# Kernel optimization log

Hardware: AMD Instinct MI355X
Metric: run time of the kernel (lower is better)

Reference implementation:

```python
import jax, jax.numpy as jnp
import numpy as np

B, T, N, E = 8, 32, 128, 2048
IN_DIM, HID, OUT = 512, 512, 512
SLOPE = 0.2  # GATConv default negative_slope


def setup_inputs() -> dict:
    key = jax.random.key(0)
    ks = jax.random.split(key, 12)
    x = jax.random.normal(ks[0], (B, T, N, IN_DIM), jnp.float32)
    edge_index = jax.random.randint(ks[1], (B, T, 2, E), 0, N)
    valid_step_index = jax.random.randint(ks[2], (B,), 1, T + 1)
    def lin(k, o, i):
        return jax.random.normal(k, (o, i), jnp.float32) / np.sqrt(i).astype(np.float32)
    W1 = lin(ks[3], HID, IN_DIM)
    a1_src = jax.random.normal(ks[4], (HID,), jnp.float32) / np.sqrt(HID).astype(np.float32)
    a1_dst = jax.random.normal(ks[5], (HID,), jnp.float32) / np.sqrt(HID).astype(np.float32)
    b1 = jnp.zeros((HID,), jnp.float32)
    W2 = lin(ks[6], OUT, HID)
    a2_src = jax.random.normal(ks[7], (OUT,), jnp.float32) / np.sqrt(OUT).astype(np.float32)
    a2_dst = jax.random.normal(ks[8], (OUT,), jnp.float32) / np.sqrt(OUT).astype(np.float32)
    b2 = jnp.zeros((OUT,), jnp.float32)
    W_time = jax.random.normal(ks[9], (T, T), jnp.float32) / np.sqrt(T).astype(np.float32)
    b_time = jnp.zeros((T,), jnp.float32)
    return dict(x=x, edge_index=edge_index, valid_step_index=valid_step_index,
                W1=W1, a1_src=a1_src, a1_dst=a1_dst, b1=b1,
                W2=W2, a2_src=a2_src, a2_dst=a2_dst, b2=b2,
                W_time=W_time, b_time=b_time)


def _gat(x, src, dst, W, a_src, a_dst, b):
    # Single-head PyG GATConv (concat=True, heads=1), self-loops already appended.
    n = x.shape[0]
    h = x @ W.T                                             # [N, H]
    e = jax.nn.leaky_relu((h @ a_src)[src] + (h @ a_dst)[dst], SLOPE)  # [E]
    m = jax.ops.segment_max(e, dst, num_segments=n)
    m = jnp.where(jnp.isfinite(m), m, 0.0)
    p = jnp.exp(e - m[dst])
    denom = jax.ops.segment_sum(p, dst, num_segments=n)
    alpha = p / denom[dst]                                  # segment softmax over incoming edges
    return jax.ops.segment_sum(h[src] * alpha[:, None], dst, num_segments=n) + b


def reference(x, edge_index, valid_step_index, W1, a1_src, a1_dst, b1,
              W2, a2_src, a2_dst, b2, W_time, b_time):
    b_, t_, n_, _ = x.shape
    g = b_ * t_
    xf = x.reshape(g, n_, -1)
    ei = edge_index.reshape(g, 2, -1)
    # add self loops (PyG GATConv default add_self_loops=True)
    loops = jnp.broadcast_to(jnp.arange(n_)[None, None, :], (g, 2, n_))
    ei = jnp.concatenate([ei, loops], axis=-1)
    src, dst = ei[:, 0], ei[:, 1]
    gat = jax.vmap(_gat, in_axes=(0, 0, 0, None, None, None, None))
    h = jax.nn.gelu(gat(xf, src, dst, W1, a1_src, a1_dst, b1), approximate=False)
    # F.dropout(p=0.2) is identity in eval mode
    h = gat(h, src, dst, W2, a2_src, a2_dst, b2)
    y = h.reshape(b_, t_, n_, -1)
    mask = (jnp.arange(t_)[None, :] < valid_step_index[:, None]).astype(y.dtype)
    y = y * mask[:, :, None, None]
    # TemporalConv: Conv2d(T, T, 1) over time-as-channel = linear mix across time, then GELU, residual
    fused = jax.nn.gelu(jnp.einsum('ts,bsnf->btnf', W_time, y)
                        + b_time[None, :, None, None], approximate=False)
    return fused + y
```

## Files before the change

kernel.cpp:

```cpp
#include <hip/hip_runtime.h>

using u16 = unsigned short;
using u32 = unsigned int;

typedef __bf16 bf16x8 __attribute__((ext_vector_type(8)));
typedef float  f32x4  __attribute__((ext_vector_type(4)));

__device__ __forceinline__ u16 f2bf(float f) {
    u32 u = __float_as_uint(f);
    u32 r = u + 0x7fffu + ((u >> 16) & 1u);
    return (u16)(r >> 16);
}
__device__ __forceinline__ float gelu_f(float x) {
    return 0.5f * x * (1.0f + erff(x * 0.70710678118654752440f));
}

#define GLOAD16(gp, lp) __builtin_amdgcn_global_load_lds( \
    (const __attribute__((address_space(1))) void*)(gp),  \
    (__attribute__((address_space(3))) void*)(lp), 16, 0, 0)

__global__ __launch_bounds__(256) void prep_kernel(
    const float* __restrict__ x, u16* __restrict__ Xb, float* __restrict__ Z)
{
    const int i0 = blockIdx.x * 256 + threadIdx.x;
    const int stride = gridDim.x * 256;
    if (i0 < 32768) ((float4*)Z)[i0] = make_float4(0.f, 0.f, 0.f, 0.f);
    for (int i = i0; i < 4194304; i += stride) {
        float4 v = ((const float4*)x)[i];
        ushort4 o;
        o.x = f2bf(v.x); o.y = f2bf(v.y); o.z = f2bf(v.z); o.w = f2bf(v.w);
        ((ushort4*)Xb)[i] = o;
    }
}

__global__ __launch_bounds__(512) void gat_gemm(
    const u16* __restrict__ A, const float* __restrict__ W,
    const float* __restrict__ a_s, const float* __restrict__ a_d,
    u16* __restrict__ HT, float* __restrict__ SS, float* __restrict__ SD)
{
    __shared__ __align__(16) u16 As[2][128 * 32];
    __shared__ float sA[128], dA[128];

    const int tid  = threadIdx.x;
    const int lane = tid & 63;
    const int w    = tid >> 6;
    const int rl   = lane & 15;
    const int grp  = lane >> 4;
    const int g    = blockIdx.x >> 1;
    const int hf   = blockIdx.x & 1;

    if (tid < 128) { sA[tid] = 0.f; dA[tid] = 0.f; }

    const u16* Ag   = A + (size_t)g * 65536;
    const u16* asrc = Ag + (size_t)(w * 16 + (lane >> 2)) * 512 + (lane & 3) * 8;
    const float* wg = W + (size_t)(hf * 256 + w * 32 + rl) * 512 + grp * 8;

    float4 wf0[2], wf1[2];
    wf0[0] = *(const float4*)&wg[0];     wf1[0] = *(const float4*)&wg[4];
    wf0[1] = *(const float4*)&wg[8192];  wf1[1] = *(const float4*)&wg[8192 + 4];

    GLOAD16(asrc, &As[0][w * 512]);
    __syncthreads();

    f32x4 acc[8][2] = {};
    int buf = 0;
    for (int kt = 0; kt < 16; ++kt) {
        if (kt < 15) GLOAD16(asrc + (kt + 1) * 32, &As[buf ^ 1][w * 512]);
        bf16x8 wb[2];
        #pragma unroll
        for (int j = 0; j < 2; ++j) {
            float4 lo = wf0[j], hi = wf1[j];
            wb[j][0] = (__bf16)lo.x; wb[j][1] = (__bf16)lo.y;
            wb[j][2] = (__bf16)lo.z; wb[j][3] = (__bf16)lo.w;
            wb[j][4] = (__bf16)hi.x; wb[j][5] = (__bf16)hi.y;
            wb[j][6] = (__bf16)hi.z; wb[j][7] = (__bf16)hi.w;
        }
        if (kt < 15) {
            #pragma unroll
            for (int j = 0; j < 2; ++j) {
                wf0[j] = *(const float4*)&wg[j * 8192 + (kt + 1) * 32];
                wf1[j] = *(const float4*)&wg[j * 8192 + (kt + 1) * 32 + 4];
            }
        }
        #pragma unroll
        for (int i = 0; i < 8; ++i) {
            bf16x8 af = *(const bf16x8*)&As[buf][(i * 16 + rl) * 32 + grp * 8];
            acc[i][0] = __builtin_amdgcn_mfma_f32_16x16x32_bf16(af, wb[0], acc[i][0], 0, 0, 0);
            acc[i][1] = __builtin_amdgcn_mfma_f32_16x16x32_bf16(af, wb[1], acc[i][1], 0, 0, 0);
        }
        __syncthreads();
        buf ^= 1;
    }

    float asv[2], adv[2];
    #pragma unroll
    for (int j = 0; j < 2; ++j) {
        int f = hf * 256 + w * 32 + j * 16 + rl;
        asv[j] = a_s[f]; adv[j] = a_d[f];
    }
    u16* Hg = HT + (size_t)g * 65536;
    #pragma unroll
    for (int i = 0; i < 8; ++i) {
        #pragma unroll
        for (int j = 0; j < 2; ++j) {
            int f = hf * 256 + w * 32 + j * 16 + rl;
            int node0 = i * 16 + grp * 4;
            ushort4 o;
            o.x = f2bf(acc[i][j][0]); o.y = f2bf(acc[i][j][1]);
            o.z = f2bf(acc[i][j][2]); o.w = f2bf(acc[i][j][3]);
            *(ushort4*)&Hg[(size_t)f * 128 + node0] = o;
        }
        #pragma unroll
        for (int r = 0; r < 4; ++r) {
            float s = acc[i][0][r] * asv[0] + acc[i][1][r] * asv[1];
            float d = acc[i][0][r] * adv[0] + acc[i][1][r] * adv[1];
            #pragma unroll
            for (int off = 1; off < 16; off <<= 1) {
                s += __shfl_xor(s, off);
                d += __shfl_xor(d, off);
            }
            if (rl == 0) {
                int node = i * 16 + grp * 4 + r;
                atomicAdd(&sA[node], s);
                atomicAdd(&dA[node], d);
            }
        }
    }
    __syncthreads();
    if (tid < 128) {
        atomicAdd(&SS[g * 128 + tid], sA[tid]);
        atomicAdd(&SD[g * 128 + tid], dA[tid]);
    }
}

template<int MODE>
__global__ __launch_bounds__(512) void gat_agg(
    const u16* __restrict__ HT, const int* __restrict__ ei,
    const float* __restrict__ SS, const float* __restrict__ SD,
    const float* __restrict__ bias, const int* __restrict__ valid,
    u16* __restrict__ outU, float* __restrict__ outF)
{
    __shared__ u16 Hts[65536];
    __shared__ u32 cntw[2048];
    __shared__ float stf[512];

    const int tid  = threadIdx.x;
    const int lane = tid & 63;
    const int w    = tid >> 6;
    const int rl   = lane & 15;
    const int grp  = lane >> 4;
    const int g    = blockIdx.x;
    const int bb   = g >> 5, tt = g & 31;

    const int4* es = (const int4*)(ei + (size_t)g * 4096);
    int4 e0 = es[tid], e1 = es[512 + tid];

    const u16* Hg = HT + (size_t)g * 65536;
    #pragma unroll
    for (int it = 0; it < 16; ++it) {
        int f = it * 32 + (tid >> 4);
        int blk = tid & 15;
        GLOAD16(Hg + (size_t)f * 128 + ((blk ^ (f & 15)) * 8), &Hts[it * 4096 + w * 512]);
    }

    for (int i = tid; i < 2048; i += 512) cntw[i] = 0u;
    if (tid < 128) {
        stf[tid]       = SS[g * 128 + tid];
        stf[128 + tid] = SD[g * 128 + tid];
    }
    __syncthreads();

    atomicAdd(&cntw[e1.x * 16 + (e0.x >> 3)], 1u << ((e0.x & 7) * 4));
    atomicAdd(&cntw[e1.y * 16 + (e0.y >> 3)], 1u << ((e0.y & 7) * 4));
    atomicAdd(&cntw[e1.z * 16 + (e0.z >> 3)], 1u << ((e0.z & 7) * 4));
    atomicAdd(&cntw[e1.w * 16 + (e0.w >> 3)], 1u << ((e0.w & 7) * 4));
    if (tid < 128) atomicAdd(&cntw[tid * 16 + (tid >> 3)], 1u << ((tid & 7) * 4));
    __syncthreads();

    for (int r = 0; r < 16; ++r) {
        int m = w * 16 + r;
        float sdm = stf[128 + m];
        u32 w0 = cntw[m * 16 + (lane >> 3)];
        u32 w1 = cntw[m * 16 + 8 + (lane >> 3)];
        u32 c0 = (w0 >> ((lane & 7) * 4)) & 15u;
        u32 c1 = (w1 >> ((lane & 7) * 4)) & 15u;
        float E0 = stf[lane] + sdm;      E0 = E0 > 0.f ? E0 : 0.2f * E0;
        float E1 = stf[lane + 64] + sdm; E1 = E1 > 0.f ? E1 : 0.2f * E1;
        float mx = fmaxf(c0 ? E0 : -1e30f, c1 ? E1 : -1e30f);
        #pragma unroll
        for (int off = 1; off < 64; off <<= 1) mx = fmaxf(mx, __shfl_xor(mx, off));
        float p = (c0 ? (float)c0 * __expf(E0 - mx) : 0.f)
                + (c1 ? (float)c1 * __expf(E1 - mx) : 0.f);
        #pragma unroll
        for (int off = 1; off < 64; off <<= 1) p += __shfl_xor(p, off);
        if (lane == 0) { stf[256 + m] = mx; stf[384 + m] = 1.f / p; }
    }
    __syncthreads();

    const int m = w * 16 + rl;
    const float sdm = stf[128 + m], Mm = stf[256 + m], rDm = stf[384 + m];
    bf16x8 pa[4];
    #pragma unroll
    for (int kb = 0; kb < 4; ++kb) {
        u32 word = cntw[m * 16 + kb * 4 + grp];
        #pragma unroll
        for (int e = 0; e < 8; ++e) {
            u32 c = (word >> (e * 4)) & 15u;
            int s = kb * 32 + grp * 8 + e;
            float ev = stf[s] + sdm; ev = ev > 0.f ? ev : 0.2f * ev;
            float p = c ? (float)c * __expf(ev - Mm) * rDm : 0.f;
            pa[kb][e] = (__bf16)p;
        }
    }

    const float msk = (MODE == 1) ? ((tt < valid[bb]) ? 1.f : 0.f) : 1.f;
    #pragma unroll 1
    for (int jc = 0; jc < 8; ++jc) {
        f32x4 acc2[4] = {};
        #pragma unroll
        for (int j4 = 0; j4 < 4; ++j4) {
            int f = jc * 64 + j4 * 16 + rl;
            #pragma unroll
            for (int kb = 0; kb < 4; ++kb) {
                bf16x8 hb = *(const bf16x8*)&Hts[f * 128 + (((kb * 4 + grp) ^ (f & 15)) * 8)];
                acc2[j4] = __builtin_amdgcn_mfma_f32_16x16x32_bf16(pa[kb], hb, acc2[j4], 0, 0, 0);
            }
        }
        #pragma unroll
        for (int j4 = 0; j4 < 4; ++j4) {
            int f = jc * 64 + j4 * 16 + rl;
            float bv = bias[f];
            #pragma unroll
            for (int r = 0; r < 4; ++r) {
                int m2 = w * 16 + grp * 4 + r;
                if (MODE == 0)
                    outU[(size_t)g * 65536 + m2 * 512 + f] = f2bf(gelu_f(acc2[j4][r] + bv));
                else
                    outF[(size_t)g * 65536 + m2 * 512 + f] = (acc2[j4][r] + bv) * msk;
            }
        }
    }
}

__global__ __launch_bounds__(256) void timemix_kernel(float* __restrict__ y,
                                                      const float* __restrict__ Wt,
                                                      const float* __restrict__ bt) {
    __shared__ float wsm[1024];
    __shared__ float bts[32];
    int tid = threadIdx.x;
    for (int i = tid; i < 1024; i += 256) wsm[i] = Wt[i];
    if (tid < 32) bts[tid] = bt[tid];
    __syncthreads();
    int blk = blockIdx.x;
    int b = blk >> 8;
    int rem = blk & 255;
    int n = rem >> 1;
    int f = (rem & 1) * 256 + tid;
    size_t base = ((size_t)b * 4096 + n) * 512 + f;
    float ys[32];
    #pragma unroll
    for (int s = 0; s < 32; ++s) ys[s] = y[base + (size_t)s * 65536];
    #pragma unroll
    for (int t = 0; t < 32; ++t) {
        float a = bts[t];
        #pragma unroll
        for (int s = 0; s < 32; ++s) a += wsm[t * 32 + s] * ys[s];
        y[base + (size_t)t * 65536] = gelu_f(a) + ys[t];
    }
}

extern "C" void kernel_launch(void* const* d_in, const int* in_sizes, int n_in,
                              void* d_out, int out_size, void* d_ws, size_t ws_size,
                              hipStream_t stream) {
    const float* x     = (const float*)d_in[0];
    const int*   ei    = (const int*)d_in[1];
    const int*   valid = (const int*)d_in[2];
    const float* W1    = (const float*)d_in[3];
    const float* a1s   = (const float*)d_in[4];
    const float* a1d   = (const float*)d_in[5];
    const float* b1    = (const float*)d_in[6];
    const float* W2    = (const float*)d_in[7];
    const float* a2s   = (const float*)d_in[8];
    const float* a2d   = (const float*)d_in[9];
    const float* b2    = (const float*)d_in[10];
    const float* Wt    = (const float*)d_in[11];
    const float* bt    = (const float*)d_in[12];
    float* out = (float*)d_out;

    char* ws = (char*)d_ws;
    u16* Xb    = (u16*)(ws);
    u16* HTb   = (u16*)(ws + 33554432);
    float* SS1 = (float*)(ws + 67108864);
    float* SD1 = (float*)(ws + 67239936);
    float* SS2 = (float*)(ws + 67371008);
    float* SD2 = (float*)(ws + 67502080);

    prep_kernel<<<2048, 256, 0, stream>>>(x, Xb, SS1);

    gat_gemm<<<512, 512, 0, stream>>>(Xb, W1, a1s, a1d, HTb, SS1, SD1);
    gat_agg<0><<<256, 512, 0, stream>>>(HTb, ei, SS1, SD1, b1, nullptr, Xb, nullptr);

    gat_gemm<<<512, 512, 0, stream>>>(Xb, W2, a2s, a2d, HTb, SS2, SD2);
    gat_agg<1><<<256, 512, 0, stream>>>(HTb, ei, SS2, SD2, b2, valid, nullptr, out);

    timemix_kernel<<<2048, 256, 0, stream>>>(out, Wt, bt);
}
```

Measured before the change: 220.2 us.

## Pre-convert weights to bf16 and retile GAT GEMM into 128x128 LDS tiles

Weights W1/W2 are now converted to bf16 once in the prep kernel, so the GEMM no longer reads fp32 weights and converts them inside its loop. The GEMM is restructured from 512-thread blocks covering 128 nodes by 256 features, with weights held in registers, into 256-thread blocks computing 128x128 tiles. Both A and B are staged in LDS, and each wave computes a 64x64 subtile of 4x4 MFMAs. This raises MFMA reuse per LDS fragment load, but it drops the double buffering, so global loads are no longer overlapped with compute and each k-step needs two barriers.

```diff
diff --git a/kernel.cpp b/kernel.cpp
--- a/kernel.cpp
+++ b/kernel.cpp
@@ -20,91 +20,93 @@
     (__attribute__((address_space(3))) void*)(lp), 16, 0, 0)
 
 __global__ __launch_bounds__(256) void prep_kernel(
-    const float* __restrict__ x, u16* __restrict__ Xb, float* __restrict__ Z)
+    const float* __restrict__ x, const float* __restrict__ W1, const float* __restrict__ W2,
+    u16* __restrict__ Xb, u16* __restrict__ W1b, u16* __restrict__ W2b,
+    float* __restrict__ Z)
 {
     const int i0 = blockIdx.x * 256 + threadIdx.x;
     const int stride = gridDim.x * 256;
     if (i0 < 32768) ((float4*)Z)[i0] = make_float4(0.f, 0.f, 0.f, 0.f);
+    for (int i = i0; i < 65536; i += stride) {
+        float4 v = ((const float4*)W1)[i];
+        ushort4 o; o.x = f2bf(v.x); o.y = f2bf(v.y); o.z = f2bf(v.z); o.w = f2bf(v.w);
+        ((ushort4*)W1b)[i] = o;
+    }
+    for (int i = i0; i < 65536; i += stride) {
+        float4 v = ((const float4*)W2)[i];
+        ushort4 o; o.x = f2bf(v.x); o.y = f2bf(v.y); o.z = f2bf(v.z); o.w = f2bf(v.w);
+        ((ushort4*)W2b)[i] = o;
+    }
     for (int i = i0; i < 4194304; i += stride) {
         float4 v = ((const float4*)x)[i];
-        ushort4 o;
-        o.x = f2bf(v.x); o.y = f2bf(v.y); o.z = f2bf(v.z); o.w = f2bf(v.w);
+        ushort4 o; o.x = f2bf(v.x); o.y = f2bf(v.y); o.z = f2bf(v.z); o.w = f2bf(v.w);
         ((ushort4*)Xb)[i] = o;
     }
 }
 
-__global__ __launch_bounds__(512) void gat_gemm(
-    const u16* __restrict__ A, const float* __restrict__ W,
+__global__ __launch_bounds__(256) void gat_gemm(
+    const u16* __restrict__ A, const u16* __restrict__ Wb,
     const float* __restrict__ a_s, const float* __restrict__ a_d,
     u16* __restrict__ HT, float* __restrict__ SS, float* __restrict__ SD)
 {
-    __shared__ __align__(16) u16 As[2][128 * 32];
+    __shared__ __align__(16) u16 As[128 * 32];
+    __shared__ __align__(16) u16 Bs[128 * 32];
     __shared__ float sA[128], dA[128];
 
     const int tid  = threadIdx.x;
     const int lane = tid & 63;
     const int w    = tid >> 6;
-    const int rl   = lane & 15;
+    const int wm   = w & 1, wn = w >> 1;
+    const int fr   = lane & 15;
     const int grp  = lane >> 4;
-    const int g    = blockIdx.x >> 1;
-    const int hf   = blockIdx.x & 1;
+    const int ko   = grp * 8;
+    const int g    = blockIdx.x >> 2;
+    const int tn   = (blockIdx.x & 3) * 128;
 
     if (tid < 128) { sA[tid] = 0.f; dA[tid] = 0.f; }
 
-    const u16* Ag   = A + (size_t)g * 65536;
-    const u16* asrc = Ag + (size_t)(w * 16 + (lane >> 2)) * 512 + (lane & 3) * 8;
-    const float* wg = W + (size_t)(hf * 256 + w * 32 + rl) * 512 + grp * 8;
-
-    float4 wf0[2], wf1[2];
-    wf0[0] = *(const float4*)&wg[0];     wf1[0] = *(const float4*)&wg[4];
-    wf0[1] = *(const float4*)&wg[8192];  wf1[1] = *(const float4*)&wg[8192 + 4];
-
-    GLOAD16(asrc, &As[0][w * 512]);
-    __syncthreads();
-
-    f32x4 acc[8][2] = {};
-    int buf = 0;
+    const int srow = lane >> 2;
+    const int skel = (lane & 3) * 8;
+    const u16* Ag0 = A  + (size_t)g * 65536 + (size_t)(w * 32 + srow) * 512 + skel;
+    const u16* Bg0 = Wb + (size_t)(tn + w * 32 + srow) * 512 + skel;
+    u16* Asl = &As[w * 1024];
+    u16* Bsl = &Bs[w * 1024];
+
+    f32x4 acc[4][4] = {};
+
     for (int kt = 0; kt < 16; ++kt) {
-        if (kt < 15) GLOAD16(asrc + (kt + 1) * 32, &As[buf ^ 1][w * 512]);
-        bf16x8 wb[2];
-        #pragma unroll
-        for (int j = 0; j < 2; ++j) {
-            float4 lo = wf0[j], hi = wf1[j];
-            wb[j][0] = (__bf16)lo.x; wb[j][1] = (__bf16)lo.y;
-            wb[j][2] = (__bf16)lo.z; wb[j][3] = (__bf16)lo.w;
-            wb[j][4] = (__bf16)hi.x; wb[j][5] = (__bf16)hi.y;
-            wb[j][6] = (__bf16)hi.z; wb[j][7] = (__bf16)hi.w;
-        }
-        if (kt < 15) {
+        GLOAD16(Ag0 + kt * 32,            Asl);
+        GLOAD16(Ag0 + 16 * 512 + kt * 32, Asl + 512);
+        GLOAD16(Bg0 + kt * 32,            Bsl);
+        GLOAD16(Bg0 + 16 * 512 + kt * 32, Bsl + 512);
+        __syncthreads();
+        bf16x8 af[4], bf[4];
+        #pragma unroll
+        for (int i = 0; i < 4; ++i) {
+            af[i] = *(const bf16x8*)&As[(wm * 64 + i * 16 + fr) * 32 + ko];
+            bf[i] = *(const bf16x8*)&Bs[(wn * 64 + i * 16 + fr) * 32 + ko];
+        }
+        #pragma unroll
+        for (int i = 0; i < 4; ++i)
             #pragma unroll
-            for (int j = 0; j < 2; ++j) {
-                wf0[j] = *(const float4*)&wg[j * 8192 + (kt + 1) * 32];
-                wf1[j] = *(const float4*)&wg[j * 8192 + (kt + 1) * 32 + 4];
-            }
-        }
-        #pragma unroll
-        for (int i = 0; i < 8; ++i) {
-            bf16x8 af = *(const bf16x8*)&As[buf][(i * 16 + rl) * 32 + grp * 8];
-            acc[i][0] = __builtin_amdgcn_mfma_f32_16x16x32_bf16(af, wb[0], acc[i][0], 0, 0, 0);
-            acc[i][1] = __builtin_amdgcn_mfma_f32_16x16x32_bf16(af, wb[1], acc[i][1], 0, 0, 0);
-        }
+            for (int j = 0; j < 4; ++j)
+                acc[i][j] = __builtin_amdgcn_mfma_f32_16x16x32_bf16(af[i], bf[j], acc[i][j], 0, 0, 0);
         __syncthreads();
-        buf ^= 1;
-    }
-
-    float asv[2], adv[2];
-    #pragma unroll
-    for (int j = 0; j < 2; ++j) {
-        int f = hf * 256 + w * 32 + j * 16 + rl;
+    }
+
+    float asv[4], adv[4];
+    #pragma unroll
+    for (int j = 0; j < 4; ++j) {
+        int f = tn + wn * 64 + j * 16 + fr;
         asv[j] = a_s[f]; adv[j] = a_d[f];
     }
     u16* Hg = HT + (size_t)g * 65536;
     #pragma unroll
-    for (int i = 0; i < 8; ++i) {
-        #pragma unroll
-        for (int j = 0; j < 2; ++j) {
-            int f = hf * 256 + w * 32 + j * 16 + rl;
-            int node0 = i * 16 + grp * 4;
+    for (int i = 0; i < 4; ++i) {
+        int node0 = wm * 64 + i * 16 + grp * 4;
+        #pragma unroll
+        for (int j = 0; j < 4; ++j) {
+            int f = tn + wn * 64 + j * 16 + fr;
             ushort4 o;
             o.x = f2bf(acc[i][j][0]); o.y = f2bf(acc[i][j][1]);
             o.z = f2bf(acc[i][j][2]); o.w = f2bf(acc[i][j][3]);
@@ -112,17 +114,18 @@
         }
         #pragma unroll
         for (int r = 0; r < 4; ++r) {
-            float s = acc[i][0][r] * asv[0] + acc[i][1][r] * asv[1];
-            float d = acc[i][0][r] * adv[0] + acc[i][1][r] * adv[1];
+            float s = acc[i][0][r] * asv[0] + acc[i][1][r] * asv[1]
+                    + acc[i][2][r] * asv[2] + acc[i][3][r] * asv[3];
+            float d = acc[i][0][r] * adv[0] + acc[i][1][r] * adv[1]
+                    + acc[i][2][r] * adv[2] + acc[i][3][r] * adv[3];
             #pragma unroll
             for (int off = 1; off < 16; off <<= 1) {
                 s += __shfl_xor(s, off);
                 d += __shfl_xor(d, off);
             }
-            if (rl == 0) {
-                int node = i * 16 + grp * 4 + r;
-                atomicAdd(&sA[node], s);
-                atomicAdd(&dA[node], d);
+            if (fr == 0) {
+                atomicAdd(&sA[node0 + r], s);
+                atomicAdd(&dA[node0 + r], d);
             }
         }
     }
@@ -290,17 +293,19 @@
     char* ws = (char*)d_ws;
     u16* Xb    = (u16*)(ws);
     u16* HTb   = (u16*)(ws + 33554432);
-    float* SS1 = (float*)(ws + 67108864);
-    float* SD1 = (float*)(ws + 67239936);
-    float* SS2 = (float*)(ws + 67371008);
-    float* SD2 = (float*)(ws + 67502080);
-
-    prep_kernel<<<2048, 256, 0, stream>>>(x, Xb, SS1);
-
-    gat_gemm<<<512, 512, 0, stream>>>(Xb, W1, a1s, a1d, HTb, SS1, SD1);
+    u16* W1b   = (u16*)(ws + 67108864);
+    u16* W2b   = (u16*)(ws + 67633152);
+    float* SS1 = (float*)(ws + 68157440);
+    float* SD1 = (float*)(ws + 68288512);
+    float* SS2 = (float*)(ws + 68419584);
+    float* SD2 = (float*)(ws + 68550656);
+
+    prep_kernel<<<2048, 256, 0, stream>>>(x, W1, W2, Xb, W1b, W2b, SS1);
+
+    gat_gemm<<<1024, 256, 0, stream>>>(Xb, W1b, a1s, a1d, HTb, SS1, SD1);
     gat_agg<0><<<256, 512, 0, stream>>>(HTb, ei, SS1, SD1, b1, nullptr, Xb, nullptr);
 
-    gat_gemm<<<512, 512, 0, stream>>>(Xb, W2, a2s, a2d, HTb, SS2, SD2);
+    gat_gemm<<<1024, 256, 0, stream>>>(Xb, W2b, a2s, a2d, HTb, SS2, SD2);
     gat_agg<1><<<256, 512, 0, stream>>>(HTb, ei, SS2, SD2, b2, valid, nullptr, out);
 
     timemix_kernel<<<2048, 256, 0, stream>>>(out, Wt, bt);
```

After: 194.8 us. 11.5% less time.
